# Optimization experiments

Hardware: AMD Instinct MI355X
Metric: run time of the kernel (lower is better)

The kernel has to match this reference:

```python
import jax, jax.numpy as jnp
import numpy as np

# Config / sizes
N = 20000       # nodes
E = 320000      # edges (avg degree 16)
IN_DIM = 6      # node feature dim
PE = 8          # laplacian PE dims
ED = 4          # edge feature dim
H = 128         # hidden dim
OUT = 4         # output dim
L = 3           # message-passing layers
T = 3           # node types (typed encoders/decoders)


def mlp(z, W1, b1, W2, b2):
    # _make_mlp: Linear -> ReLU -> Linear
    return jax.nn.relu(z @ W1 + b1) @ W2 + b2


def typed_mlp(z, W1, b1, W2, b2, types):
    # W1: [T, Din, H]; compute all T branches, select per-node by type
    h = jax.nn.relu(jnp.einsum('ni,tih->tnh', z, W1) + b1[:, None, :])
    o = jnp.einsum('tnh,tho->tno', h, W2) + b2[:, None, :]
    onehot = jax.nn.one_hot(types, W1.shape[0], dtype=o.dtype)  # [N, T]
    return jnp.einsum('tno,nt->no', o, onehot)


def setup_inputs() -> dict:
    key = jax.random.key(0)
    ks = jax.random.split(key, 40)

    def w(k, shape, fan_in):
        return jax.random.normal(k, shape, dtype=jnp.float32) / np.float32(np.sqrt(fan_in))

    inp = {}
    inp['x'] = jax.random.normal(ks[0], (N, IN_DIM), dtype=jnp.float32)
    inp['pe'] = jax.random.normal(ks[1], (N, PE), dtype=jnp.float32)
    inp['edge_attr'] = jax.random.normal(ks[2], (E, ED), dtype=jnp.float32)
    # typed node encoders: (in_dim+pe_dims) -> H -> H
    inp['enc_W1'] = w(ks[3], (T, IN_DIM + PE, H), IN_DIM + PE)
    inp['enc_b1'] = jnp.zeros((T, H), jnp.float32)
    inp['enc_W2'] = w(ks[4], (T, H, H), H)
    inp['enc_b2'] = jnp.zeros((T, H), jnp.float32)
    # edge encoder: ED -> H -> H
    inp['ee_W1'] = w(ks[5], (ED, H), ED)
    inp['ee_b1'] = jnp.zeros((H,), jnp.float32)
    inp['ee_W2'] = w(ks[6], (H, H), H)
    inp['ee_b2'] = jnp.zeros((H,), jnp.float32)
    # per-layer edge update (3H->H->H), node update (2H->H->H), fusion (H->H->H)
    inp['eu_W1'] = w(ks[7], (L, 3 * H, H), 3 * H)
    inp['eu_b1'] = jnp.zeros((L, H), jnp.float32)
    inp['eu_W2'] = w(ks[8], (L, H, H), H)
    inp['eu_b2'] = jnp.zeros((L, H), jnp.float32)
    inp['nu_W1'] = w(ks[9], (L, 2 * H, H), 2 * H)
    inp['nu_b1'] = jnp.zeros((L, H), jnp.float32)
    inp['nu_W2'] = w(ks[10], (L, H, H), H)
    inp['nu_b2'] = jnp.zeros((L, H), jnp.float32)
    inp['fu_W1'] = w(ks[11], (L, H, H), H)
    inp['fu_b1'] = jnp.zeros((L, H), jnp.float32)
    inp['fu_W2'] = w(ks[12], (L, H, H), H)
    inp['fu_b2'] = jnp.zeros((L, H), jnp.float32)
    # typed decoders: H -> H -> OUT
    inp['dec_W1'] = w(ks[13], (T, H, H), H)
    inp['dec_b1'] = jnp.zeros((T, H), jnp.float32)
    inp['dec_W2'] = w(ks[14], (T, H, OUT), H)
    inp['dec_b2'] = jnp.zeros((T, OUT), jnp.float32)
    # int inputs
    inp['edge_index'] = jax.random.randint(ks[15], (2, E), 0, N)
    inp['node_types'] = jax.random.randint(ks[16], (N,), 0, T)
    return inp


def reference(x, pe, edge_attr,
              enc_W1, enc_b1, enc_W2, enc_b2,
              ee_W1, ee_b1, ee_W2, ee_b2,
              eu_W1, eu_b1, eu_W2, eu_b2,
              nu_W1, nu_b1, nu_W2, nu_b2,
              fu_W1, fu_b1, fu_W2, fu_b2,
              dec_W1, dec_b1, dec_W2, dec_b2,
              edge_index, node_types):
    n = x.shape[0]
    src, dst = edge_index[0], edge_index[1]
    # typed node encode on [x || pe]
    h_nodes = typed_mlp(jnp.concatenate([x, pe], axis=-1),
                        enc_W1, enc_b1, enc_W2, enc_b2, node_types)
    # edge encode
    h_edges = mlp(edge_attr, ee_W1, ee_b1, ee_W2, ee_b2)
    num_layers = eu_W1.shape[0]
    for l in range(num_layers):
        # gather endpoint states, edge MLP, residual on edges
        m_edge = mlp(jnp.concatenate([h_nodes[src], h_nodes[dst], h_edges], axis=-1),
                     eu_W1[l], eu_b1[l], eu_W2[l], eu_b2[l])
        h_edges = h_edges + m_edge
        # scatter-add aggregation to destination nodes (index_add_)
        m_node = jax.ops.segment_sum(h_edges, dst, num_segments=n)
        # node update + residual, then fusion (dropout is eval/identity)
        upd = mlp(jnp.concatenate([h_nodes, m_node], axis=-1),
                  nu_W1[l], nu_b1[l], nu_W2[l], nu_b2[l])
        local = h_nodes + upd
        h_nodes = mlp(local, fu_W1[l], fu_b1[l], fu_W2[l], fu_b2[l])
    # typed decode
    out = typed_mlp(h_nodes, dec_W1, dec_b1, dec_W2, dec_b2, node_types)
    return out
```

## Files before the change

### kernel.cpp

```cpp
#include <hip/hip_runtime.h>
#include <hip/hip_bf16.h>

typedef __hip_bfloat16 bf16;
typedef __attribute__((ext_vector_type(8))) short short8;
typedef __attribute__((ext_vector_type(4))) float floatx4;

#define HDIM 128
#define NCANON 27

__device__ __forceinline__ float b2f(bf16 v) { return __bfloat162float(v); }
__device__ __forceinline__ float s2f(short s) {
  return __uint_as_float(((unsigned int)(unsigned short)s) << 16);
}
__device__ __forceinline__ short f2s(float f) {
  return (short)__bfloat16_as_ushort(__float2bfloat16(f));
}

__global__ void detect_kernel(const unsigned short* __restrict__ xraw, int* __restrict__ flag) {
  int j = threadIdx.x;
  unsigned short u = xraw[2 * j];
  int e = (u >> 7) & 0xFF;
  int ok = (u == 0) || (e >= 100 && e <= 140);
  unsigned long long m = __ballot(ok);
  if (j == 0) flag[0] = (__popcll(m) >= 48) ? 1 : 0;
}

struct CanonDesc {
  const void* src[NCANON];
  int prefix[NCANON + 1];
};

__global__ void canon_kernel(CanonDesc d, const int* __restrict__ flag,
                             bf16* __restrict__ out, int total) {
  int t = blockIdx.x * 256 + threadIdx.x;
  if (t >= total) return;
  int ti = 0;
  while (d.prefix[ti + 1] <= t) ti++;
  int off = t - d.prefix[ti];
  if (flag[0]) out[t] = ((const bf16*)d.src[ti])[off];
  else         out[t] = __float2bfloat16(((const float*)d.src[ti])[off]);
}

__global__ void emit_kernel(const bf16* __restrict__ canon_out, const int* __restrict__ flag,
                            void* __restrict__ d_out, int n) {
  int t = blockIdx.x * 256 + threadIdx.x;
  if (t >= n) return;
  if (flag[0]) ((bf16*)d_out)[t] = canon_out[t];
  else         ((float*)d_out)[t] = __bfloat162float(canon_out[t]);
}

__global__ void hist_kernel(const int* __restrict__ dst, int* __restrict__ cnt, int E) {
  int e = blockIdx.x * 256 + threadIdx.x;
  if (e < E) atomicAdd(&cnt[dst[e]], 1);
}

__global__ void scan1_kernel(const int* __restrict__ cnt, int* __restrict__ bsum, int n) {
  int tid = threadIdx.x, lane = tid & 63, wave = tid >> 6;
  int i = blockIdx.x * 256 + tid;
  int v = (i < n) ? cnt[i] : 0;
  #pragma unroll
  for (int d = 32; d; d >>= 1) v += __shfl_down(v, d);
  __shared__ int ws[4];
  if (lane == 0) ws[wave] = v;
  __syncthreads();
  if (tid == 0) bsum[blockIdx.x] = ws[0] + ws[1] + ws[2] + ws[3];
}

__global__ void scan2_kernel(int* __restrict__ bsum, int nb) {
  int lane = threadIdx.x;
  int a0 = (lane < nb) ? bsum[lane] : 0;
  int b0 = (64 + lane < nb) ? bsum[64 + lane] : 0;
  int a = a0, b = b0;
  #pragma unroll
  for (int d = 1; d < 64; d <<= 1) { int t = __shfl_up(a, d); if (lane >= d) a += t; }
  int totA = __shfl(a, 63);
  #pragma unroll
  for (int d = 1; d < 64; d <<= 1) { int t = __shfl_up(b, d); if (lane >= d) b += t; }
  int totB = __shfl(b, 63);
  if (lane < nb) bsum[lane] = a - a0;
  if (64 + lane < nb) bsum[64 + lane] = b - b0 + totA;
  if (lane == 0) bsum[nb] = totA + totB;
}

__global__ void scan3_kernel(const int* __restrict__ cnt, const int* __restrict__ bsum,
                             int* __restrict__ row_start, int n, int nb) {
  __shared__ int sh[256];
  int tid = threadIdx.x;
  int i = blockIdx.x * 256 + tid;
  int v = (i < n) ? cnt[i] : 0;
  sh[tid] = v;
  __syncthreads();
  #pragma unroll
  for (int off = 1; off < 256; off <<= 1) {
    int t = (tid >= off) ? sh[tid - off] : 0;
    __syncthreads();
    sh[tid] += t;
    __syncthreads();
  }
  if (i < n) row_start[i] = bsum[blockIdx.x] + sh[tid] - v;
  if (blockIdx.x == 0 && tid == 0) row_start[n] = bsum[nb];
}

__global__ void scatter_kernel(const int* __restrict__ src, const int* __restrict__ dst,
                               const int* __restrict__ row_start, int* __restrict__ cursor,
                               int* __restrict__ sortedE, int* __restrict__ srcS,
                               int* __restrict__ dstS, int E) {
  int e = blockIdx.x * 256 + threadIdx.x;
  if (e < E) {
    int d = dst[e];
    int pos = row_start[d] + atomicAdd(&cursor[d], 1);
    sortedE[pos] = e;
    srcS[pos] = src[e];
    dstS[pos] = d;
  }
}

__global__ void tcount_kernel(const int* __restrict__ types, int* __restrict__ bcnt, int n) {
  int i = blockIdx.x * 256 + threadIdx.x;
  int lane = threadIdx.x & 63, wave = threadIdx.x >> 6;
  int t = (i < n) ? types[i] : -1;
  __shared__ int wc[4][3];
  unsigned long long m0 = __ballot(t == 0);
  unsigned long long m1 = __ballot(t == 1);
  unsigned long long m2 = __ballot(t == 2);
  if (lane == 0) {
    wc[wave][0] = __popcll(m0); wc[wave][1] = __popcll(m1); wc[wave][2] = __popcll(m2);
  }
  __syncthreads();
  if (threadIdx.x < 3)
    bcnt[blockIdx.x * 3 + threadIdx.x] =
        wc[0][threadIdx.x] + wc[1][threadIdx.x] + wc[2][threadIdx.x] + wc[3][threadIdx.x];
}

__global__ void tscan_kernel(const int* __restrict__ bcnt, int* __restrict__ boff,
                             int* __restrict__ ts, int nb, int n) {
  int lane = threadIdx.x;
  __shared__ int tots[3];
  for (int t = 0; t < 3; t++) {
    int a0 = (lane < nb) ? bcnt[lane * 3 + t] : 0;
    int b0 = (64 + lane < nb) ? bcnt[(64 + lane) * 3 + t] : 0;
    int a = a0, b = b0;
    #pragma unroll
    for (int d = 1; d < 64; d <<= 1) { int x = __shfl_up(a, d); if (lane >= d) a += x; }
    int totA = __shfl(a, 63);
    #pragma unroll
    for (int d = 1; d < 64; d <<= 1) { int x = __shfl_up(b, d); if (lane >= d) b += x; }
    int totB = __shfl(b, 63);
    if (lane < nb) boff[lane * 3 + t] = a - a0;
    if (64 + lane < nb) boff[(64 + lane) * 3 + t] = b - b0 + totA;
    if (lane == 0) tots[t] = totA + totB;
  }
  __syncthreads();
  int tot0 = tots[0], tot1 = tots[1];
  if (lane == 0) { ts[0] = 0; ts[1] = tot0; ts[2] = tot0 + tot1; ts[3] = n; }
  for (int idx = lane; idx < nb; idx += 64) {
    boff[idx * 3 + 1] += tot0;
    boff[idx * 3 + 2] += tot0 + tot1;
  }
}

__global__ void tscatter2_kernel(const int* __restrict__ types, const int* __restrict__ boff,
                                 int* __restrict__ perm, int n) {
  int i = blockIdx.x * 256 + threadIdx.x;
  int lane = threadIdx.x & 63, wave = threadIdx.x >> 6;
  int t = (i < n) ? types[i] : -1;
  __shared__ int wc[4][3];
  unsigned long long m0 = __ballot(t == 0);
  unsigned long long m1 = __ballot(t == 1);
  unsigned long long m2 = __ballot(t == 2);
  if (lane == 0) {
    wc[wave][0] = __popcll(m0); wc[wave][1] = __popcll(m1); wc[wave][2] = __popcll(m2);
  }
  __syncthreads();
  if (i >= n) return;
  unsigned long long mt = (t == 0) ? m0 : ((t == 1) ? m1 : m2);
  unsigned long long below = (lane == 0) ? 0ull : ((1ull << lane) - 1ull);
  int laneRank = __popcll(mt & below);
  int waveOff = 0;
  for (int w = 0; w < wave; w++) waveOff += wc[w][t];
  perm[boff[blockIdx.x * 3 + t] + waveOff + laneRank] = i;
}

struct PackJob { const bf16* src; bf16* dst; int Ksrc; int KS; int srcCols; };
struct PackJobs { PackJob j[40]; };

__global__ void pack_all_kernel(PackJobs J) {
  PackJob job = J.j[blockIdx.y];
  int idx = blockIdx.x * 256 + threadIdx.x;
  int total = 8 * job.KS * 64;
  if (idx >= total) return;
  int lane = idx & 63;
  int ks = (idx >> 6) % job.KS;
  int ct = idx / (64 * job.KS);
  bf16* o = job.dst + (size_t)idx * 8;
  int ncol = ct * 16 + (lane & 15);
  int kb = ks * 32 + ((lane >> 4) & 3) * 8;
  #pragma unroll
  for (int jj = 0; jj < 8; jj++) {
    int k = kb + jj;
    o[jj] = (k < job.Ksrc && ncol < job.srcCols)
              ? job.src[(size_t)k * job.srcCols + ncol] : __float2bfloat16(0.f);
  }
}

__global__ void __launch_bounds__(256) ygemm_kernel(
    const bf16* __restrict__ X,
    const bf16* __restrict__ WpA, const bf16* __restrict__ WpB,
    bf16* __restrict__ outA, bf16* __restrict__ outB, int M) {
  const bf16* Wp = blockIdx.y ? WpB : WpA;
  bf16* outp = blockIdx.y ? outB : outA;
  constexpr int BM = 64, RT = 4, SK = 136;
  __shared__ bf16 Zt[BM * SK];
  const int tid = threadIdx.x;
  const int lane = tid & 63, wave = tid >> 6, colq = lane & 15, quad = lane >> 4;
  const int row0 = blockIdx.x * BM;
  {
    int row = tid >> 2, sub = tid & 3;
    int gr = row0 + row;
    bool ok = gr < M;
    #pragma unroll
    for (int j = 0; j < 4; j++) {
      int seg = j * 4 + sub;
      uint4 v = {0u, 0u, 0u, 0u};
      if (ok) v = *(const uint4*)(X + (size_t)gr * HDIM + seg * 8);
      *(uint4*)(&Zt[row * SK + seg * 8]) = v;
    }
  }
  __syncthreads();
  floatx4 acc[RT][2];
  #pragma unroll
  for (int rt = 0; rt < RT; rt++)
    #pragma unroll
    for (int c = 0; c < 2; c++) acc[rt][c] = (floatx4){0.f, 0.f, 0.f, 0.f};
  #pragma unroll
  for (int ks = 0; ks < 4; ks++) {
    short8 bfr0 = *(const short8*)(Wp + (((size_t)(wave * 2 + 0) * 4 + ks) * 64 + lane) * 8);
    short8 bfr1 = *(const short8*)(Wp + (((size_t)(wave * 2 + 1) * 4 + ks) * 64 + lane) * 8);
    #pragma unroll
    for (int rt = 0; rt < RT; rt++) {
      short8 a = *(const short8*)(&Zt[(rt * 16 + colq) * SK + ks * 32 + quad * 8]);
      acc[rt][0] = __builtin_amdgcn_mfma_f32_16x16x32_bf16(a, bfr0, acc[rt][0], 0, 0, 0);
      acc[rt][1] = __builtin_amdgcn_mfma_f32_16x16x32_bf16(a, bfr1, acc[rt][1], 0, 0, 0);
    }
  }
  #pragma unroll
  for (int c = 0; c < 2; c++) {
    int col = wave * 32 + c * 16 + colq;
    #pragma unroll
    for (int rt = 0; rt < RT; rt++)
      #pragma unroll
      for (int r = 0; r < 4; r++) {
        int grow = row0 + rt * 16 + quad * 4 + r;
        if (grow < M) outp[(size_t)grow * HDIM + col] = __float2bfloat16(acc[rt][c][r]);
      }
  }
}

template<int BM>
__global__ void __launch_bounds__(256) eu_kernel(
    const bf16* __restrict__ he, const bf16* __restrict__ ysrc, const bf16* __restrict__ ydst,
    const int* __restrict__ srcS, const int* __restrict__ dstS,
    const bf16* __restrict__ W1p, const bf16* __restrict__ b1v,
    const bf16* __restrict__ W2p, const bf16* __restrict__ b2v,
    bf16* __restrict__ outp, float* __restrict__ mnode, int M) {
  constexpr int RT = BM / 16;
  constexpr int SK = 264;
  __shared__ bf16 Zt[BM * SK];
  __shared__ int dstLds[BM];
  const int tid = threadIdx.x;
  const int lane = tid & 63, wave = tid >> 6, colq = lane & 15, quad = lane >> 4;
  const int row0 = blockIdx.x * BM;
  constexpr int TPR = 256 / BM;
  {
    int row = tid / TPR, sub = tid % TPR;
    int gr = row0 + row;
    bool ok = gr < M;
    int g0 = ok ? srcS[gr] : 0;
    int g1 = ok ? dstS[gr] : 0;
    if (sub == 0) dstLds[row] = ok ? g1 : -1;
    #pragma unroll
    for (int j = 0; j < 32 / TPR; j++) {
      int c = j * TPR + sub;
      int part = c >> 4, seg = c & 15;
      if (part == 0) {
        short8 o = {0, 0, 0, 0, 0, 0, 0, 0};
        if (ok) {
          short8 a = *(const short8*)(ysrc + (size_t)g0 * HDIM + seg * 8);
          short8 b = *(const short8*)(ydst + (size_t)g1 * HDIM + seg * 8);
          #pragma unroll
          for (int k = 0; k < 8; k++) o[k] = f2s(s2f(a[k]) + s2f(b[k]));
        }
        *(short8*)(&Zt[row * SK + seg * 8]) = o;
      } else {
        uint4 v = {0u, 0u, 0u, 0u};
        if (ok) v = *(const uint4*)(he + (size_t)gr * HDIM + seg * 8);
        *(uint4*)(&Zt[row * SK + 128 + seg * 8]) = v;
      }
    }
  }
  __syncthreads();

  floatx4 acc[RT][2];
  #pragma unroll
  for (int rt = 0; rt < RT; rt++)
    #pragma unroll
    for (int c = 0; c < 2; c++) acc[rt][c] = (floatx4){0.f, 0.f, 0.f, 0.f};
  #pragma unroll
  for (int ks = 0; ks < 4; ks++) {
    short8 bfr0 = *(const short8*)(W1p + (((size_t)(wave * 2 + 0) * 4 + ks) * 64 + lane) * 8);
    short8 bfr1 = *(const short8*)(W1p + (((size_t)(wave * 2 + 1) * 4 + ks) * 64 + lane) * 8);
    #pragma unroll
    for (int rt = 0; rt < RT; rt++) {
      short8 a = *(const short8*)(&Zt[(rt * 16 + colq) * SK + 128 + ks * 32 + quad * 8]);
      acc[rt][0] = __builtin_amdgcn_mfma_f32_16x16x32_bf16(a, bfr0, acc[rt][0], 0, 0, 0);
      acc[rt][1] = __builtin_amdgcn_mfma_f32_16x16x32_bf16(a, bfr1, acc[rt][1], 0, 0, 0);
    }
  }
  #pragma unroll
  for (int c = 0; c < 2; c++) {
    int col = wave * 32 + c * 16 + colq;
    float bv = b2f(b1v[col]);
    #pragma unroll
    for (int rt = 0; rt < RT; rt++)
      #pragma unroll
      for (int r = 0; r < 4; r++) {
        int lrow = rt * 16 + quad * 4 + r;
        float v = acc[rt][c][r] + bv + b2f(Zt[lrow * SK + col]);
        Zt[lrow * SK + col] = __float2bfloat16(fmaxf(v, 0.f));
      }
  }
  __syncthreads();

  floatx4 acc2[RT][2];
  #pragma unroll
  for (int rt = 0; rt < RT; rt++)
    #pragma unroll
    for (int c = 0; c < 2; c++) acc2[rt][c] = (floatx4){0.f, 0.f, 0.f, 0.f};
  #pragma unroll
  for (int ks = 0; ks < 4; ks++) {
    short8 bfr0 = *(const short8*)(W2p + (((size_t)(wave * 2 + 0) * 4 + ks) * 64 + lane) * 8);
    short8 bfr1 = *(const short8*)(W2p + (((size_t)(wave * 2 + 1) * 4 + ks) * 64 + lane) * 8);
    #pragma unroll
    for (int rt = 0; rt < RT; rt++) {
      short8 a = *(const short8*)(&Zt[(rt * 16 + colq) * SK + ks * 32 + quad * 8]);
      acc2[rt][0] = __builtin_amdgcn_mfma_f32_16x16x32_bf16(a, bfr0, acc2[rt][0], 0, 0, 0);
      acc2[rt][1] = __builtin_amdgcn_mfma_f32_16x16x32_bf16(a, bfr1, acc2[rt][1], 0, 0, 0);
    }
  }
  #pragma unroll
  for (int c = 0; c < 2; c++) {
    int col = wave * 32 + c * 16 + colq;
    float bv = b2f(b2v[col]);
    #pragma unroll
    for (int rt = 0; rt < RT; rt++)
      #pragma unroll
      for (int r = 0; r < 4; r++) {
        int lrow = rt * 16 + quad * 4 + r;
        int grow = row0 + lrow;
        float v = acc2[rt][c][r] + bv + b2f(Zt[lrow * SK + 128 + col]);
        bf16 vb = __float2bfloat16(v);
        Zt[lrow * SK + 128 + col] = vb;
        if (grow < M) outp[(size_t)grow * HDIM + col] = vb;
      }
  }
  __syncthreads();

  if (tid < 128) {
    int col = tid;
    float s = 0.f;
    int runDst = dstLds[0];
    bool touchStart = true;
    for (int r = 0; r < BM; r++) {
      int d = dstLds[r];
      if (d != runDst) {
        if (runDst >= 0) {
          float* mp = &mnode[(size_t)runDst * HDIM + col];
          if (touchStart) atomicAdd(mp, s); else *mp = s;
        }
        runDst = d; s = 0.f; touchStart = false;
      }
      s += b2f(Zt[r * SK + 128 + col]);
    }
    if (runDst >= 0) atomicAdd(&mnode[(size_t)runDst * HDIM + col], s);
  }
}

__global__ void __launch_bounds__(256) node_kernel(
    const bf16* __restrict__ h_nodes, const float* __restrict__ mnode,
    const bf16* __restrict__ nuW1, const bf16* __restrict__ nuB1,
    const bf16* __restrict__ nuW2, const bf16* __restrict__ nuB2,
    const bf16* __restrict__ fuW1, const bf16* __restrict__ fuB1,
    const bf16* __restrict__ fuW2, const bf16* __restrict__ fuB2,
    bf16* __restrict__ outp, int M) {
  constexpr int BM = 64, RT = 4, SK = 264;
  __shared__ bf16 Zt[BM * SK];
  const int tid = threadIdx.x;
  const int lane = tid & 63, wave = tid >> 6, colq = lane & 15, quad = lane >> 4;
  const int row0 = blockIdx.x * BM;
  {
    int row = tid >> 2, sub = tid & 3;
    int gr = row0 + row;
    bool ok = gr < M;
    #pragma unroll
    for (int j = 0; j < 8; j++) {
      int c = j * 4 + sub;
      int part = c >> 4, seg = c & 15;
      if (part == 0) {
        uint4 v = {0u, 0u, 0u, 0u};
        if (ok) v = *(const uint4*)(h_nodes + (size_t)gr * HDIM + seg * 8);
        *(uint4*)(&Zt[row * SK + seg * 8]) = v;
      } else {
        short8 o = {0, 0, 0, 0, 0, 0, 0, 0};
        if (ok) {
          const float* mp = mnode + (size_t)gr * HDIM + seg * 8;
          #pragma unroll
          for (int k = 0; k < 8; k++) o[k] = f2s(mp[k]);
        }
        *(short8*)(&Zt[row * SK + 128 + seg * 8]) = o;
      }
    }
  }
  __syncthreads();

  floatx4 acc[RT][2];
  #pragma unroll
  for (int rt = 0; rt < RT; rt++)
    #pragma unroll
    for (int c = 0; c < 2; c++) acc[rt][c] = (floatx4){0.f, 0.f, 0.f, 0.f};
  #pragma unroll
  for (int ks = 0; ks < 8; ks++) {
    short8 bfr0 = *(const short8*)(nuW1 + (((size_t)(wave * 2 + 0) * 8 + ks) * 64 + lane) * 8);
    short8 bfr1 = *(const short8*)(nuW1 + (((size_t)(wave * 2 + 1) * 8 + ks) * 64 + lane) * 8);
    #pragma unroll
    for (int rt = 0; rt < RT; rt++) {
      short8 a = *(const short8*)(&Zt[(rt * 16 + colq) * SK + ks * 32 + quad * 8]);
      acc[rt][0] = __builtin_amdgcn_mfma_f32_16x16x32_bf16(a, bfr0, acc[rt][0], 0, 0, 0);
      acc[rt][1] = __builtin_amdgcn_mfma_f32_16x16x32_bf16(a, bfr1, acc[rt][1], 0, 0, 0);
    }
  }
  __syncthreads();
  #pragma unroll
  for (int c = 0; c < 2; c++) {
    int col = wave * 32 + c * 16 + colq;
    float bv = b2f(nuB1[col]);
    #pragma unroll
    for (int rt = 0; rt < RT; rt++)
      #pragma unroll
      for (int r = 0; r < 4; r++)
        Zt[(rt * 16 + quad * 4 + r) * SK + 128 + col] =
            __float2bfloat16(fmaxf(acc[rt][c][r] + bv, 0.f));
  }
  __syncthreads();

  #pragma unroll
  for (int rt = 0; rt < RT; rt++)
    #pragma unroll
    for (int c = 0; c < 2; c++) acc[rt][c] = (floatx4){0.f, 0.f, 0.f, 0.f};
  #pragma unroll
  for (int ks = 0; ks < 4; ks++) {
    short8 bfr0 = *(const short8*)(nuW2 + (((size_t)(wave * 2 + 0) * 4 + ks) * 64 + lane) * 8);
    short8 bfr1 = *(const short8*)(nuW2 + (((size_t)(wave * 2 + 1) * 4 + ks) * 64 + lane) * 8);
    #pragma unroll
    for (int rt = 0; rt < RT; rt++) {
      short8 a = *(const short8*)(&Zt[(rt * 16 + colq) * SK + 128 + ks * 32 + quad * 8]);
      acc[rt][0] = __builtin_amdgcn_mfma_f32_16x16x32_bf16(a, bfr0, acc[rt][0], 0, 0, 0);
      acc[rt][1] = __builtin_amdgcn_mfma_f32_16x16x32_bf16(a, bfr1, acc[rt][1], 0, 0, 0);
    }
  }
  #pragma unroll
  for (int c = 0; c < 2; c++) {
    int col = wave * 32 + c * 16 + colq;
    float bv = b2f(nuB2[col]);
    #pragma unroll
    for (int rt = 0; rt < RT; rt++)
      #pragma unroll
      for (int r = 0; r < 4; r++) {
        int lrow = rt * 16 + quad * 4 + r;
        float v = acc[rt][c][r] + bv + b2f(Zt[lrow * SK + col]);
        Zt[lrow * SK + col] = __float2bfloat16(v);
      }
  }
  __syncthreads();

  #pragma unroll
  for (int rt = 0; rt < RT; rt++)
    #pragma unroll
    for (int c = 0; c < 2; c++) acc[rt][c] = (floatx4){0.f, 0.f, 0.f, 0.f};
  #pragma unroll
  for (int ks = 0; ks < 4; ks++) {
    short8 bfr0 = *(const short8*)(fuW1 + (((size_t)(wave * 2 + 0) * 4 + ks) * 64 + lane) * 8);
    short8 bfr1 = *(const short8*)(fuW1 + (((size_t)(wave * 2 + 1) * 4 + ks) * 64 + lane) * 8);
    #pragma unroll
    for (int rt = 0; rt < RT; rt++) {
      short8 a = *(const short8*)(&Zt[(rt * 16 + colq) * SK + ks * 32 + quad * 8]);
      acc[rt][0] = __builtin_amdgcn_mfma_f32_16x16x32_bf16(a, bfr0, acc[rt][0], 0, 0, 0);
      acc[rt][1] = __builtin_amdgcn_mfma_f32_16x16x32_bf16(a, bfr1, acc[rt][1], 0, 0, 0);
    }
  }
  #pragma unroll
  for (int c = 0; c < 2; c++) {
    int col = wave * 32 + c * 16 + colq;
    float bv = b2f(fuB1[col]);
    #pragma unroll
    for (int rt = 0; rt < RT; rt++)
      #pragma unroll
      for (int r = 0; r < 4; r++)
        Zt[(rt * 16 + quad * 4 + r) * SK + 128 + col] =
            __float2bfloat16(fmaxf(acc[rt][c][r] + bv, 0.f));
  }
  __syncthreads();

  #pragma unroll
  for (int rt = 0; rt < RT; rt++)
    #pragma unroll
    for (int c = 0; c < 2; c++) acc[rt][c] = (floatx4){0.f, 0.f, 0.f, 0.f};
  #pragma unroll
  for (int ks = 0; ks < 4; ks++) {
    short8 bfr0 = *(const short8*)(fuW2 + (((size_t)(wave * 2 + 0) * 4 + ks) * 64 + lane) * 8);
    short8 bfr1 = *(const short8*)(fuW2 + (((size_t)(wave * 2 + 1) * 4 + ks) * 64 + lane) * 8);
    #pragma unroll
    for (int rt = 0; rt < RT; rt++) {
      short8 a = *(const short8*)(&Zt[(rt * 16 + colq) * SK + 128 + ks * 32 + quad * 8]);
      acc[rt][0] = __builtin_amdgcn_mfma_f32_16x16x32_bf16(a, bfr0, acc[rt][0], 0, 0, 0);
      acc[rt][1] = __builtin_amdgcn_mfma_f32_16x16x32_bf16(a, bfr1, acc[rt][1], 0, 0, 0);
    }
  }
  #pragma unroll
  for (int c = 0; c < 2; c++) {
    int col = wave * 32 + c * 16 + colq;
    float bv = b2f(fuB2[col]);
    #pragma unroll
    for (int rt = 0; rt < RT; rt++)
      #pragma unroll
      for (int r = 0; r < 4; r++) {
        int grow = row0 + rt * 16 + quad * 4 + r;
        if (grow < M) outp[(size_t)grow * HDIM + col] = __float2bfloat16(acc[rt][c][r] + bv);
      }
  }
}

template<int KS1, bool DEC>
__global__ void __launch_bounds__(256) typed_kernel(
    const bf16* __restrict__ in0, const bf16* __restrict__ in1,
    const int* __restrict__ perm, const int* __restrict__ ts,
    const bf16* __restrict__ W1p, int w1s, const bf16* __restrict__ b1v, int b1s,
    const bf16* __restrict__ W2p, int w2s, const bf16* __restrict__ b2v, int b2s,
    bf16* __restrict__ outp) {
  constexpr int BM = 64, RT = 4;
  constexpr int SK = KS1 * 32 + 8;
  constexpr int HS = 136;
  int t = blockIdx.y;
  int rs = ts[t], re = ts[t + 1];
  int row0 = rs + blockIdx.x * BM;
  if (row0 >= re) return;
  __shared__ bf16 Zt[BM * SK];
  __shared__ bf16 Hid[BM * HS];
  __shared__ int gIdx[BM];
  const int tid = threadIdx.x;
  const int lane = tid & 63, wave = tid >> 6, colq = lane & 15, quad = lane >> 4;
  for (int i = tid; i < BM; i += 256) gIdx[i] = (row0 + i < re) ? perm[row0 + i] : -1;
  __syncthreads();
  if (DEC) {
    int row = tid >> 2, sub = tid & 3;
    int g = gIdx[row];
    #pragma unroll
    for (int j = 0; j < 4; j++) {
      int seg = j * 4 + sub;
      uint4 v = {0u, 0u, 0u, 0u};
      if (g >= 0) v = *(const uint4*)(in0 + (size_t)g * HDIM + seg * 8);
      *(uint4*)(&Zt[row * SK + seg * 8]) = v;
    }
  } else {
    for (int i = tid; i < BM * 32; i += 256) {
      int row = i >> 5, k = i & 31;
      int g = gIdx[row];
      bf16 v = __float2bfloat16(0.f);
      if (g >= 0 && k < 14) v = (k < 6) ? in0[(size_t)g * 6 + k] : in1[(size_t)g * 8 + (k - 6)];
      Zt[row * SK + k] = v;
    }
  }
  __syncthreads();

  const bf16* W1t = W1p + (size_t)t * w1s;
  const bf16* W2t = W2p + (size_t)t * w2s;
  floatx4 acc[RT][2];
  #pragma unroll
  for (int rt = 0; rt < RT; rt++)
    #pragma unroll
    for (int c = 0; c < 2; c++) acc[rt][c] = (floatx4){0.f, 0.f, 0.f, 0.f};
  #pragma unroll
  for (int ks = 0; ks < KS1; ks++) {
    short8 bfr0 = *(const short8*)(W1t + (((size_t)(wave * 2 + 0) * KS1 + ks) * 64 + lane) * 8);
    short8 bfr1 = *(const short8*)(W1t + (((size_t)(wave * 2 + 1) * KS1 + ks) * 64 + lane) * 8);
    #pragma unroll
    for (int rt = 0; rt < RT; rt++) {
      short8 a = *(const short8*)(&Zt[(rt * 16 + colq) * SK + ks * 32 + quad * 8]);
      acc[rt][0] = __builtin_amdgcn_mfma_f32_16x16x32_bf16(a, bfr0, acc[rt][0], 0, 0, 0);
      acc[rt][1] = __builtin_amdgcn_mfma_f32_16x16x32_bf16(a, bfr1, acc[rt][1], 0, 0, 0);
    }
  }
  #pragma unroll
  for (int c = 0; c < 2; c++) {
    int col = wave * 32 + c * 16 + colq;
    float bv = b2f(b1v[t * b1s + col]);
    #pragma unroll
    for (int rt = 0; rt < RT; rt++)
      #pragma unroll
      for (int r = 0; r < 4; r++) {
        float v = acc[rt][c][r] + bv;
        Hid[(rt * 16 + quad * 4 + r) * HS + col] = __float2bfloat16(fmaxf(v, 0.f));
      }
  }
  __syncthreads();

  floatx4 acc2[RT][2];
  #pragma unroll
  for (int rt = 0; rt < RT; rt++)
    #pragma unroll
    for (int c = 0; c < 2; c++) acc2[rt][c] = (floatx4){0.f, 0.f, 0.f, 0.f};
  #pragma unroll
  for (int ks = 0; ks < 4; ks++) {
    short8 bfr0 = *(const short8*)(W2t + (((size_t)(wave * 2 + 0) * 4 + ks) * 64 + lane) * 8);
    short8 bfr1 = *(const short8*)(W2t + (((size_t)(wave * 2 + 1) * 4 + ks) * 64 + lane) * 8);
    #pragma unroll
    for (int rt = 0; rt < RT; rt++) {
      short8 a = *(const short8*)(&Hid[(rt * 16 + colq) * HS + ks * 32 + quad * 8]);
      acc2[rt][0] = __builtin_amdgcn_mfma_f32_16x16x32_bf16(a, bfr0, acc2[rt][0], 0, 0, 0);
      acc2[rt][1] = __builtin_amdgcn_mfma_f32_16x16x32_bf16(a, bfr1, acc2[rt][1], 0, 0, 0);
    }
  }
  if (DEC) {
    if (wave == 0 && colq < 4) {
      float bv = b2f(b2v[t * b2s + colq]);
      #pragma unroll
      for (int rt = 0; rt < RT; rt++)
        #pragma unroll
        for (int r = 0; r < 4; r++) {
          int g = gIdx[rt * 16 + quad * 4 + r];
          if (g >= 0) outp[(size_t)g * 4 + colq] = __float2bfloat16(acc2[rt][0][r] + bv);
        }
    }
  } else {
    #pragma unroll
    for (int c = 0; c < 2; c++) {
      int col = wave * 32 + c * 16 + colq;
      float bv = b2f(b2v[t * b2s + col]);
      #pragma unroll
      for (int rt = 0; rt < RT; rt++)
        #pragma unroll
        for (int r = 0; r < 4; r++) {
          int g = gIdx[rt * 16 + quad * 4 + r];
          if (g >= 0) outp[(size_t)g * HDIM + col] = __float2bfloat16(acc2[rt][c][r] + bv);
        }
    }
  }
}

template<int BM>
__global__ void __launch_bounds__(256) ee_kernel(
    const bf16* __restrict__ p0, const int* __restrict__ idx0,
    const bf16* __restrict__ W1p, const bf16* __restrict__ b1v,
    const bf16* __restrict__ W2p, const bf16* __restrict__ b2v,
    bf16* __restrict__ outp, int M) {
  constexpr int RT = BM / 16;
  constexpr int SK = 136;
  __shared__ bf16 Zt[BM * SK];
  const int tid = threadIdx.x;
  const int lane = tid & 63, wave = tid >> 6, colq = lane & 15, quad = lane >> 4;
  const int row0 = blockIdx.x * BM;

  for (int i = tid; i < BM * 4; i += 256) {
    int row = i >> 2, seg = i & 3;
    int gr = row0 + row;
    uint4 val = {0u, 0u, 0u, 0u};
    if (seg == 0 && gr < M) {
      int g = idx0 ? idx0[gr] : gr;
      uint2 v = *(const uint2*)(p0 + (size_t)g * 4);
      val.x = v.x; val.y = v.y;
    }
    *(uint4*)(&Zt[row * SK + seg * 8]) = val;
  }
  __syncthreads();

  floatx4 acc[RT][2];
  #pragma unroll
  for (int rt = 0; rt < RT; rt++)
    #pragma unroll
    for (int c = 0; c < 2; c++) acc[rt][c] = (floatx4){0.f, 0.f, 0.f, 0.f};
  {
    short8 bfr0 = *(const short8*)(W1p + (((size_t)(wave * 2 + 0)) * 64 + lane) * 8);
    short8 bfr1 = *(const short8*)(W1p + (((size_t)(wave * 2 + 1)) * 64 + lane) * 8);
    #pragma unroll
    for (int rt = 0; rt < RT; rt++) {
      short8 a = *(const short8*)(&Zt[(rt * 16 + colq) * SK + quad * 8]);
      acc[rt][0] = __builtin_amdgcn_mfma_f32_16x16x32_bf16(a, bfr0, acc[rt][0], 0, 0, 0);
      acc[rt][1] = __builtin_amdgcn_mfma_f32_16x16x32_bf16(a, bfr1, acc[rt][1], 0, 0, 0);
    }
  }
  __syncthreads();
  #pragma unroll
  for (int c = 0; c < 2; c++) {
    int col = wave * 32 + c * 16 + colq;
    float bv = b2f(b1v[col]);
    #pragma unroll
    for (int rt = 0; rt < RT; rt++)
      #pragma unroll
      for (int r = 0; r < 4; r++)
        Zt[(rt * 16 + quad * 4 + r) * SK + col] =
            __float2bfloat16(fmaxf(acc[rt][c][r] + bv, 0.f));
  }
  __syncthreads();

  floatx4 acc2[RT][2];
  #pragma unroll
  for (int rt = 0; rt < RT; rt++)
    #pragma unroll
    for (int c = 0; c < 2; c++) acc2[rt][c] = (floatx4){0.f, 0.f, 0.f, 0.f};
  #pragma unroll
  for (int ks = 0; ks < 4; ks++) {
    short8 bfr0 = *(const short8*)(W2p + (((size_t)(wave * 2 + 0) * 4 + ks) * 64 + lane) * 8);
    short8 bfr1 = *(const short8*)(W2p + (((size_t)(wave * 2 + 1) * 4 + ks) * 64 + lane) * 8);
    #pragma unroll
    for (int rt = 0; rt < RT; rt++) {
      short8 a = *(const short8*)(&Zt[(rt * 16 + colq) * SK + ks * 32 + quad * 8]);
      acc2[rt][0] = __builtin_amdgcn_mfma_f32_16x16x32_bf16(a, bfr0, acc2[rt][0], 0, 0, 0);
      acc2[rt][1] = __builtin_amdgcn_mfma_f32_16x16x32_bf16(a, bfr1, acc2[rt][1], 0, 0, 0);
    }
  }
  #pragma unroll
  for (int c = 0; c < 2; c++) {
    int col = wave * 32 + c * 16 + colq;
    float bv = b2f(b2v[col]);
    #pragma unroll
    for (int rt = 0; rt < RT; rt++)
      #pragma unroll
      for (int r = 0; r < 4; r++) {
        int grow = row0 + rt * 16 + quad * 4 + r;
        if (grow < M)
          outp[(size_t)grow * HDIM + col] = __float2bfloat16(acc2[rt][c][r] + bv);
      }
  }
}

extern "C" void kernel_launch(void* const* d_in, const int* in_sizes, int n_in,
                              void* d_out, int out_size, void* d_ws, size_t ws_size,
                              hipStream_t stream) {
  const int* edge_index = (const int*)d_in[27];
  const int* node_types = (const int*)d_in[28];
  const int N = in_sizes[28];
  const int E = in_sizes[2] / 4;
  const int L = in_sizes[12] / HDIM;
  const int* srcI = edge_index;
  const int* dstI = edge_index + E;

  CanonDesc cd;
  int total = 0;
  for (int i = 0; i < NCANON; i++) { cd.src[i] = d_in[i]; cd.prefix[i] = total; total += in_sizes[i]; }
  cd.prefix[NCANON] = total;

  char* wsb = (char*)d_ws;
  size_t off = 0;
  auto alloc = [&](size_t bytes) -> void* {
    void* p = wsb + off;
    off += (bytes + 255) & ~(size_t)255;
    return p;
  };
  int*  flag      = (int*)alloc(256);
  bf16* arena     = (bf16*)alloc((size_t)total * 2);
  bf16* h_nodes   = (bf16*)alloc((size_t)N * HDIM * 2);
  bf16* h_edges   = (bf16*)alloc((size_t)E * HDIM * 2);
  float* m_node   = (float*)alloc((size_t)N * HDIM * 4);
  bf16* ysrcb     = (bf16*)alloc((size_t)N * HDIM * 2);
  bf16* ydstb     = (bf16*)alloc((size_t)N * HDIM * 2);
  bf16* canon_out = (bf16*)alloc((size_t)out_size * 2);
  int* counts     = (int*)alloc((size_t)N * 4);
  int* cursor     = (int*)alloc((size_t)N * 4);
  int* row_start  = (int*)alloc((size_t)(N + 1) * 4);
  int* bsum       = (int*)alloc(260 * 4);
  int* sortedE    = (int*)alloc((size_t)E * 4);
  int* srcS       = (int*)alloc((size_t)E * 4);
  int* dstS       = (int*)alloc((size_t)E * 4);
  int* bcntT      = (int*)alloc(512 * 4);
  int* boffT      = (int*)alloc(512 * 4);
  int* tsArr      = (int*)alloc(64);
  int* permT      = (int*)alloc((size_t)N * 4);
  bf16* eeW1p  = (bf16*)alloc(4096 * 2);
  bf16* eeW2p  = (bf16*)alloc(16384 * 2);
  bf16* encW1p = (bf16*)alloc(3 * 4096 * 2);
  bf16* encW2p = (bf16*)alloc(3 * 16384 * 2);
  bf16* decW1p = (bf16*)alloc(3 * 16384 * 2);
  bf16* decW2p = (bf16*)alloc(3 * 16384 * 2);
  bf16* euW1a  = (bf16*)alloc((size_t)L * 16384 * 2);
  bf16* euW1b  = (bf16*)alloc((size_t)L * 16384 * 2);
  bf16* euW1c  = (bf16*)alloc((size_t)L * 16384 * 2);
  bf16* euW2p  = (bf16*)alloc((size_t)L * 16384 * 2);
  bf16* nuW1p  = (bf16*)alloc((size_t)L * 32768 * 2);
  bf16* nuW2p  = (bf16*)alloc((size_t)L * 16384 * 2);
  bf16* fuW1p  = (bf16*)alloc((size_t)L * 16384 * 2);
  bf16* fuW2p  = (bf16*)alloc((size_t)L * 16384 * 2);

  const bf16* cX     = arena + cd.prefix[0];
  const bf16* cPE    = arena + cd.prefix[1];
  const bf16* cEA    = arena + cd.prefix[2];
  const bf16* cEncW1 = arena + cd.prefix[3];
  const bf16* cEncB1 = arena + cd.prefix[4];
  const bf16* cEncW2 = arena + cd.prefix[5];
  const bf16* cEncB2 = arena + cd.prefix[6];
  const bf16* cEeW1  = arena + cd.prefix[7];
  const bf16* cEeB1  = arena + cd.prefix[8];
  const bf16* cEeW2  = arena + cd.prefix[9];
  const bf16* cEeB2  = arena + cd.prefix[10];
  const bf16* cEuW1  = arena + cd.prefix[11];
  const bf16* cEuB1  = arena + cd.prefix[12];
  const bf16* cEuW2  = arena + cd.prefix[13];
  const bf16* cEuB2  = arena + cd.prefix[14];
  const bf16* cNuW1  = arena + cd.prefix[15];
  const bf16* cNuB1  = arena + cd.prefix[16];
  const bf16* cNuW2  = arena + cd.prefix[17];
  const bf16* cNuB2  = arena + cd.prefix[18];
  const bf16* cFuW1  = arena + cd.prefix[19];
  const bf16* cFuB1  = arena + cd.prefix[20];
  const bf16* cFuW2  = arena + cd.prefix[21];
  const bf16* cFuB2  = arena + cd.prefix[22];
  const bf16* cDecW1 = arena + cd.prefix[23];
  const bf16* cDecB1 = arena + cd.prefix[24];
  const bf16* cDecW2 = arena + cd.prefix[25];
  const bf16* cDecB2 = arena + cd.prefix[26];

  detect_kernel<<<1, 64, 0, stream>>>((const unsigned short*)d_in[0], flag);
  canon_kernel<<<(total + 255) / 256, 256, 0, stream>>>(cd, flag, arena, total);

  hipMemsetAsync(counts, 0, (size_t)N * 4, stream);
  hipMemsetAsync(cursor, 0, (size_t)N * 4, stream);

  PackJobs PJ;
  int nj = 0;
  PJ.j[nj++] = {cEeW1, eeW1p, 4, 1, 128};
  PJ.j[nj++] = {cEeW2, eeW2p, 128, 4, 128};
  for (int l = 0; l < L; l++) {
    const bf16* w1 = cEuW1 + (size_t)l * 384 * HDIM;
    PJ.j[nj++] = {w1,                 euW1a + (size_t)l * 16384, 128, 4, 128};
    PJ.j[nj++] = {w1 + 128 * HDIM,    euW1b + (size_t)l * 16384, 128, 4, 128};
    PJ.j[nj++] = {w1 + 256 * HDIM,    euW1c + (size_t)l * 16384, 128, 4, 128};
    PJ.j[nj++] = {cEuW2 + (size_t)l * HDIM * HDIM, euW2p + (size_t)l * 16384, 128, 4, 128};
    PJ.j[nj++] = {cNuW1 + (size_t)l * 256 * HDIM,  nuW1p + (size_t)l * 32768, 256, 8, 128};
    PJ.j[nj++] = {cNuW2 + (size_t)l * HDIM * HDIM, nuW2p + (size_t)l * 16384, 128, 4, 128};
    PJ.j[nj++] = {cFuW1 + (size_t)l * HDIM * HDIM, fuW1p + (size_t)l * 16384, 128, 4, 128};
    PJ.j[nj++] = {cFuW2 + (size_t)l * HDIM * HDIM, fuW2p + (size_t)l * 16384, 128, 4, 128};
  }
  for (int t = 0; t < 3; t++) {
    PJ.j[nj++] = {cEncW1 + (size_t)t * 14 * HDIM,   encW1p + (size_t)t * 4096, 14, 1, 128};
    PJ.j[nj++] = {cEncW2 + (size_t)t * HDIM * HDIM, encW2p + (size_t)t * 16384, 128, 4, 128};
    PJ.j[nj++] = {cDecW1 + (size_t)t * HDIM * HDIM, decW1p + (size_t)t * 16384, 128, 4, 128};
    PJ.j[nj++] = {cDecW2 + (size_t)t * HDIM * 4,    decW2p + (size_t)t * 16384, 128, 4, 4};
  }
  pack_all_kernel<<<dim3(16, nj), 256, 0, stream>>>(PJ);

  int nb = (N + 255) / 256;
  hist_kernel<<<(E + 255) / 256, 256, 0, stream>>>(dstI, counts, E);
  scan1_kernel<<<nb, 256, 0, stream>>>(counts, bsum, N);
  scan2_kernel<<<1, 64, 0, stream>>>(bsum, nb);
  scan3_kernel<<<nb, 256, 0, stream>>>(counts, bsum, row_start, N, nb);
  scatter_kernel<<<(E + 255) / 256, 256, 0, stream>>>(srcI, dstI, row_start, cursor,
                                                      sortedE, srcS, dstS, E);
  tcount_kernel<<<nb, 256, 0, stream>>>(node_types, bcntT, N);
  tscan_kernel<<<1, 64, 0, stream>>>(bcntT, boffT, tsArr, nb, N);
  tscatter2_kernel<<<nb, 256, 0, stream>>>(node_types, boffT, permT, N);

  int ngrid64 = (N + 63) / 64;
  typed_kernel<1, false><<<dim3(ngrid64, 3), 256, 0, stream>>>(
      cX, cPE, permT, tsArr, encW1p, 4096, cEncB1, HDIM,
      encW2p, 16384, cEncB2, HDIM, h_nodes);

  int egrid32  = (E + 31) / 32;
  int egrid128 = (E + 127) / 128;

  ee_kernel<128><<<egrid128, 256, 0, stream>>>(
      cEA, sortedE, eeW1p, cEeB1, eeW2p, cEeB2, h_edges, E);

  for (int l = 0; l < L; l++) {
    hipMemsetAsync(m_node, 0, (size_t)N * HDIM * 4, stream);
    ygemm_kernel<<<dim3(ngrid64, 2), 256, 0, stream>>>(
        h_nodes, euW1a + (size_t)l * 16384, euW1b + (size_t)l * 16384, ysrcb, ydstb, N);
    eu_kernel<32><<<egrid32, 256, 0, stream>>>(
        h_edges, ysrcb, ydstb, srcS, dstS,
        euW1c + (size_t)l * 16384, cEuB1 + l * HDIM,
        euW2p + (size_t)l * 16384, cEuB2 + l * HDIM, h_edges, m_node, E);
    node_kernel<<<ngrid64, 256, 0, stream>>>(
        h_nodes, m_node,
        nuW1p + (size_t)l * 32768, cNuB1 + l * HDIM,
        nuW2p + (size_t)l * 16384, cNuB2 + l * HDIM,
        fuW1p + (size_t)l * 16384, cFuB1 + l * HDIM,
        fuW2p + (size_t)l * 16384, cFuB2 + l * HDIM, h_nodes, N);
  }

  typed_kernel<4, true><<<dim3(ngrid64, 3), 256, 0, stream>>>(
      h_nodes, nullptr, permT, tsArr, decW1p, 16384, cDecB1, HDIM,
      decW2p, 16384, cDecB2, 4, canon_out);
  emit_kernel<<<(out_size + 255) / 256, 256, 0, stream>>>(canon_out, flag, d_out, out_size);
  (void)n_in; (void)ws_size;
}
```

Baseline: 503.8 us.

## Fuse small setup kernels, fold memset into ygemm, store projections in fp32

Several small launches go away. Format detection moves into the canon kernel, the three type-sort kernels become one single-block sort, the emit kernel becomes a direct dtype-aware write from the decoder, and the per-layer m_node memset is folded into ygemm. The ygemm outputs change from bf16 to fp32, which doubles the gather traffic in eu_kernel but avoids a double rounding. The segment reduction in eu_kernel now uses all 256 threads split into two halves of rows. The single-block type sort serialises about 20 iterations with syncs.

```diff
diff --git a/kernel.cpp b/kernel.cpp
--- a/kernel.cpp
+++ b/kernel.cpp
@@ -14,15 +14,6 @@
 }
 __device__ __forceinline__ short f2s(float f) {
   return (short)__bfloat16_as_ushort(__float2bfloat16(f));
-}
-
-__global__ void detect_kernel(const unsigned short* __restrict__ xraw, int* __restrict__ flag) {
-  int j = threadIdx.x;
-  unsigned short u = xraw[2 * j];
-  int e = (u >> 7) & 0xFF;
-  int ok = (u == 0) || (e >= 100 && e <= 140);
-  unsigned long long m = __ballot(ok);
-  if (j == 0) flag[0] = (__popcll(m) >= 48) ? 1 : 0;
 }
 
 struct CanonDesc {
@@ -30,23 +21,27 @@
   int prefix[NCANON + 1];
 };
 
-__global__ void canon_kernel(CanonDesc d, const int* __restrict__ flag,
-                             bf16* __restrict__ out, int total) {
-  int t = blockIdx.x * 256 + threadIdx.x;
+__global__ void canon_kernel(CanonDesc d, const unsigned short* __restrict__ xraw,
+                             int* __restrict__ flagOut, bf16* __restrict__ out, int total) {
+  __shared__ int sflag;
+  int tid = threadIdx.x;
+  if (tid < 64) {
+    unsigned short u = xraw[2 * tid];
+    int e = (u >> 7) & 0xFF;
+    int ok = (u == 0) || (e >= 100 && e <= 140);
+    unsigned long long m = __ballot(ok);
+    if (tid == 0) sflag = (__popcll(m) >= 48) ? 1 : 0;
+  }
+  __syncthreads();
+  int isBf = sflag;
+  if (blockIdx.x == 0 && tid == 0) flagOut[0] = isBf;
+  int t = blockIdx.x * 256 + tid;
   if (t >= total) return;
-  int ti = 0;
-  while (d.prefix[ti + 1] <= t) ti++;
-  int off = t - d.prefix[ti];
-  if (flag[0]) out[t] = ((const bf16*)d.src[ti])[off];
-  else         out[t] = __float2bfloat16(((const float*)d.src[ti])[off]);
-}
-
-__global__ void emit_kernel(const bf16* __restrict__ canon_out, const int* __restrict__ flag,
-                            void* __restrict__ d_out, int n) {
-  int t = blockIdx.x * 256 + threadIdx.x;
-  if (t >= n) return;
-  if (flag[0]) ((bf16*)d_out)[t] = canon_out[t];
-  else         ((float*)d_out)[t] = __bfloat162float(canon_out[t]);
+  int lo = 0, hi = NCANON;
+  while (lo + 1 < hi) { int mid = (lo + hi) >> 1; if (d.prefix[mid] <= t) lo = mid; else hi = mid; }
+  int off = t - d.prefix[lo];
+  out[t] = isBf ? ((const bf16*)d.src[lo])[off]
+                : __float2bfloat16(((const float*)d.src[lo])[off]);
 }
 
 __global__ void hist_kernel(const int* __restrict__ dst, int* __restrict__ cnt, int E) {
@@ -115,70 +110,54 @@
   }
 }
 
-__global__ void tcount_kernel(const int* __restrict__ types, int* __restrict__ bcnt, int n) {
-  int i = blockIdx.x * 256 + threadIdx.x;
-  int lane = threadIdx.x & 63, wave = threadIdx.x >> 6;
-  int t = (i < n) ? types[i] : -1;
-  __shared__ int wc[4][3];
-  unsigned long long m0 = __ballot(t == 0);
-  unsigned long long m1 = __ballot(t == 1);
-  unsigned long long m2 = __ballot(t == 2);
-  if (lane == 0) {
-    wc[wave][0] = __popcll(m0); wc[wave][1] = __popcll(m1); wc[wave][2] = __popcll(m2);
-  }
-  __syncthreads();
-  if (threadIdx.x < 3)
-    bcnt[blockIdx.x * 3 + threadIdx.x] =
-        wc[0][threadIdx.x] + wc[1][threadIdx.x] + wc[2][threadIdx.x] + wc[3][threadIdx.x];
-}
-
-__global__ void tscan_kernel(const int* __restrict__ bcnt, int* __restrict__ boff,
-                             int* __restrict__ ts, int nb, int n) {
-  int lane = threadIdx.x;
-  __shared__ int tots[3];
-  for (int t = 0; t < 3; t++) {
-    int a0 = (lane < nb) ? bcnt[lane * 3 + t] : 0;
-    int b0 = (64 + lane < nb) ? bcnt[(64 + lane) * 3 + t] : 0;
-    int a = a0, b = b0;
-    #pragma unroll
-    for (int d = 1; d < 64; d <<= 1) { int x = __shfl_up(a, d); if (lane >= d) a += x; }
-    int totA = __shfl(a, 63);
-    #pragma unroll
-    for (int d = 1; d < 64; d <<= 1) { int x = __shfl_up(b, d); if (lane >= d) b += x; }
-    int totB = __shfl(b, 63);
-    if (lane < nb) boff[lane * 3 + t] = a - a0;
-    if (64 + lane < nb) boff[(64 + lane) * 3 + t] = b - b0 + totA;
-    if (lane == 0) tots[t] = totA + totB;
-  }
-  __syncthreads();
-  int tot0 = tots[0], tot1 = tots[1];
-  if (lane == 0) { ts[0] = 0; ts[1] = tot0; ts[2] = tot0 + tot1; ts[3] = n; }
-  for (int idx = lane; idx < nb; idx += 64) {
-    boff[idx * 3 + 1] += tot0;
-    boff[idx * 3 + 2] += tot0 + tot1;
-  }
-}
-
-__global__ void tscatter2_kernel(const int* __restrict__ types, const int* __restrict__ boff,
-                                 int* __restrict__ perm, int n) {
-  int i = blockIdx.x * 256 + threadIdx.x;
-  int lane = threadIdx.x & 63, wave = threadIdx.x >> 6;
-  int t = (i < n) ? types[i] : -1;
-  __shared__ int wc[4][3];
-  unsigned long long m0 = __ballot(t == 0);
-  unsigned long long m1 = __ballot(t == 1);
-  unsigned long long m2 = __ballot(t == 2);
-  if (lane == 0) {
-    wc[wave][0] = __popcll(m0); wc[wave][1] = __popcll(m1); wc[wave][2] = __popcll(m2);
-  }
-  __syncthreads();
-  if (i >= n) return;
-  unsigned long long mt = (t == 0) ? m0 : ((t == 1) ? m1 : m2);
-  unsigned long long below = (lane == 0) ? 0ull : ((1ull << lane) - 1ull);
-  int laneRank = __popcll(mt & below);
-  int waveOff = 0;
-  for (int w = 0; w < wave; w++) waveOff += wc[w][t];
-  perm[boff[blockIdx.x * 3 + t] + waveOff + laneRank] = i;
+__global__ void __launch_bounds__(1024) tsort_kernel(const int* __restrict__ types,
+                                                     int* __restrict__ ts,
+                                                     int* __restrict__ perm, int n) {
+  __shared__ int wc[16][3];
+  __shared__ int base[3];
+  int tid = threadIdx.x, lane = tid & 63, wave = tid >> 6;
+  int c0 = 0, c1 = 0, c2 = 0;
+  for (int i = tid; i < n; i += 1024) {
+    int t = types[i];
+    c0 += (t == 0); c1 += (t == 1); c2 += (t == 2);
+  }
+  #pragma unroll
+  for (int d = 32; d; d >>= 1) {
+    c0 += __shfl_down(c0, d); c1 += __shfl_down(c1, d); c2 += __shfl_down(c2, d);
+  }
+  if (lane == 0) { wc[wave][0] = c0; wc[wave][1] = c1; wc[wave][2] = c2; }
+  __syncthreads();
+  if (tid == 0) {
+    int t0 = 0, t1 = 0;
+    for (int w = 0; w < 16; w++) { t0 += wc[w][0]; t1 += wc[w][1]; }
+    ts[0] = 0; ts[1] = t0; ts[2] = t0 + t1; ts[3] = n;
+    base[0] = 0; base[1] = t0; base[2] = t0 + t1;
+  }
+  __syncthreads();
+  for (int i0 = 0; i0 < n; i0 += 1024) {
+    int i = i0 + tid;
+    int t = (i < n) ? types[i] : -1;
+    unsigned long long m0 = __ballot(t == 0);
+    unsigned long long m1 = __ballot(t == 1);
+    unsigned long long m2 = __ballot(t == 2);
+    if (lane == 0) { wc[wave][0] = __popcll(m0); wc[wave][1] = __popcll(m1); wc[wave][2] = __popcll(m2); }
+    __syncthreads();
+    if (i < n) {
+      unsigned long long mt = (t == 0) ? m0 : ((t == 1) ? m1 : m2);
+      unsigned long long below = (lane == 0) ? 0ull : ((1ull << lane) - 1ull);
+      int r = __popcll(mt & below);
+      int woff = 0;
+      for (int w = 0; w < wave; w++) woff += wc[w][t];
+      perm[base[t] + woff + r] = i;
+    }
+    __syncthreads();
+    if (tid == 0) {
+      int a0 = 0, a1 = 0, a2 = 0;
+      for (int w = 0; w < 16; w++) { a0 += wc[w][0]; a1 += wc[w][1]; a2 += wc[w][2]; }
+      base[0] += a0; base[1] += a1; base[2] += a2;
+    }
+    __syncthreads();
+  }
 }
 
 struct PackJob { const bf16* src; bf16* dst; int Ksrc; int KS; int srcCols; };
@@ -206,14 +185,23 @@
 __global__ void __launch_bounds__(256) ygemm_kernel(
     const bf16* __restrict__ X,
     const bf16* __restrict__ WpA, const bf16* __restrict__ WpB,
-    bf16* __restrict__ outA, bf16* __restrict__ outB, int M) {
+    float* __restrict__ outA, float* __restrict__ outB,
+    float* __restrict__ mnode, int M) {
   const bf16* Wp = blockIdx.y ? WpB : WpA;
-  bf16* outp = blockIdx.y ? outB : outA;
+  float* outp = blockIdx.y ? outB : outA;
   constexpr int BM = 64, RT = 4, SK = 136;
   __shared__ bf16 Zt[BM * SK];
   const int tid = threadIdx.x;
   const int lane = tid & 63, wave = tid >> 6, colq = lane & 15, quad = lane >> 4;
   const int row0 = blockIdx.x * BM;
+  if (blockIdx.y == 0) {
+    float4 z = {0.f, 0.f, 0.f, 0.f};
+    for (int i = tid; i < BM * 32; i += 256) {
+      int row = i >> 5, q = i & 31;
+      int gr = row0 + row;
+      if (gr < M) *(float4*)(mnode + (size_t)gr * HDIM + q * 4) = z;
+    }
+  }
   {
     int row = tid >> 2, sub = tid & 3;
     int gr = row0 + row;
@@ -251,14 +239,14 @@
       #pragma unroll
       for (int r = 0; r < 4; r++) {
         int grow = row0 + rt * 16 + quad * 4 + r;
-        if (grow < M) outp[(size_t)grow * HDIM + col] = __float2bfloat16(acc[rt][c][r]);
+        if (grow < M) outp[(size_t)grow * HDIM + col] = acc[rt][c][r];
       }
   }
 }
 
 template<int BM>
 __global__ void __launch_bounds__(256) eu_kernel(
-    const bf16* __restrict__ he, const bf16* __restrict__ ysrc, const bf16* __restrict__ ydst,
+    const bf16* __restrict__ he, const float* __restrict__ ysrc, const float* __restrict__ ydst,
     const int* __restrict__ srcS, const int* __restrict__ dstS,
     const bf16* __restrict__ W1p, const bf16* __restrict__ b1v,
     const bf16* __restrict__ W2p, const bf16* __restrict__ b2v,
@@ -285,10 +273,10 @@
       if (part == 0) {
         short8 o = {0, 0, 0, 0, 0, 0, 0, 0};
         if (ok) {
-          short8 a = *(const short8*)(ysrc + (size_t)g0 * HDIM + seg * 8);
-          short8 b = *(const short8*)(ydst + (size_t)g1 * HDIM + seg * 8);
+          const float* ap = ysrc + (size_t)g0 * HDIM + seg * 8;
+          const float* bp = ydst + (size_t)g1 * HDIM + seg * 8;
           #pragma unroll
-          for (int k = 0; k < 8; k++) o[k] = f2s(s2f(a[k]) + s2f(b[k]));
+          for (int k = 0; k < 8; k++) o[k] = f2s(ap[k] + bp[k]);
         }
         *(short8*)(&Zt[row * SK + seg * 8]) = o;
       } else {
@@ -365,12 +353,14 @@
   }
   __syncthreads();
 
-  if (tid < 128) {
-    int col = tid;
+  {
+    int col = tid & 127;
+    int half = tid >> 7;
+    int rbeg = half * (BM / 2), rend = rbeg + (BM / 2);
     float s = 0.f;
-    int runDst = dstLds[0];
+    int runDst = dstLds[rbeg];
     bool touchStart = true;
-    for (int r = 0; r < BM; r++) {
+    for (int r = rbeg; r < rend; r++) {
       int d = dstLds[r];
       if (d != runDst) {
         if (runDst >= 0) {
@@ -542,10 +532,10 @@
 template<int KS1, bool DEC>
 __global__ void __launch_bounds__(256) typed_kernel(
     const bf16* __restrict__ in0, const bf16* __restrict__ in1,
-    const int* __restrict__ perm, const int* __restrict__ ts,
+    const int* __restrict__ perm, const int* __restrict__ ts, const int* __restrict__ flagp,
     const bf16* __restrict__ W1p, int w1s, const bf16* __restrict__ b1v, int b1s,
     const bf16* __restrict__ W2p, int w2s, const bf16* __restrict__ b2v, int b2s,
-    bf16* __restrict__ outp) {
+    void* __restrict__ outp) {
   constexpr int BM = 64, RT = 4;
   constexpr int SK = KS1 * 32 + 8;
   constexpr int HS = 136;
@@ -631,13 +621,18 @@
   }
   if (DEC) {
     if (wave == 0 && colq < 4) {
+      int isBf = flagp[0];
       float bv = b2f(b2v[t * b2s + colq]);
       #pragma unroll
       for (int rt = 0; rt < RT; rt++)
         #pragma unroll
         for (int r = 0; r < 4; r++) {
           int g = gIdx[rt * 16 + quad * 4 + r];
-          if (g >= 0) outp[(size_t)g * 4 + colq] = __float2bfloat16(acc2[rt][0][r] + bv);
+          if (g >= 0) {
+            float v = acc2[rt][0][r] + bv;
+            if (isBf) ((bf16*)outp)[(size_t)g * 4 + colq] = __float2bfloat16(v);
+            else      ((float*)outp)[(size_t)g * 4 + colq] = v;
+          }
         }
     }
   } else {
@@ -650,7 +645,7 @@
         #pragma unroll
         for (int r = 0; r < 4; r++) {
           int g = gIdx[rt * 16 + quad * 4 + r];
-          if (g >= 0) outp[(size_t)g * HDIM + col] = __float2bfloat16(acc2[rt][c][r] + bv);
+          if (g >= 0) ((bf16*)outp)[(size_t)g * HDIM + col] = __float2bfloat16(acc2[rt][c][r] + bv);
         }
     }
   }
@@ -770,9 +765,8 @@
   bf16* h_nodes   = (bf16*)alloc((size_t)N * HDIM * 2);
   bf16* h_edges   = (bf16*)alloc((size_t)E * HDIM * 2);
   float* m_node   = (float*)alloc((size_t)N * HDIM * 4);
-  bf16* ysrcb     = (bf16*)alloc((size_t)N * HDIM * 2);
-  bf16* ydstb     = (bf16*)alloc((size_t)N * HDIM * 2);
-  bf16* canon_out = (bf16*)alloc((size_t)out_size * 2);
+  float* ysrcb    = (float*)alloc((size_t)N * HDIM * 4);
+  float* ydstb    = (float*)alloc((size_t)N * HDIM * 4);
   int* counts     = (int*)alloc((size_t)N * 4);
   int* cursor     = (int*)alloc((size_t)N * 4);
   int* row_start  = (int*)alloc((size_t)(N + 1) * 4);
@@ -780,8 +774,6 @@
   int* sortedE    = (int*)alloc((size_t)E * 4);
   int* srcS       = (int*)alloc((size_t)E * 4);
   int* dstS       = (int*)alloc((size_t)E * 4);
-  int* bcntT      = (int*)alloc(512 * 4);
-  int* boffT      = (int*)alloc(512 * 4);
   int* tsArr      = (int*)alloc(64);
   int* permT      = (int*)alloc((size_t)N * 4);
   bf16* eeW1p  = (bf16*)alloc(4096 * 2);
@@ -827,8 +819,8 @@
   const bf16* cDecW2 = arena + cd.prefix[25];
   const bf16* cDecB2 = arena + cd.prefix[26];
 
-  detect_kernel<<<1, 64, 0, stream>>>((const unsigned short*)d_in[0], flag);
-  canon_kernel<<<(total + 255) / 256, 256, 0, stream>>>(cd, flag, arena, total);
+  canon_kernel<<<(total + 255) / 256, 256, 0, stream>>>(
+      cd, (const unsigned short*)d_in[0], flag, arena, total);
 
   hipMemsetAsync(counts, 0, (size_t)N * 4, stream);
   hipMemsetAsync(cursor, 0, (size_t)N * 4, stream);
@@ -863,13 +855,11 @@
   scan3_kernel<<<nb, 256, 0, stream>>>(counts, bsum, row_start, N, nb);
   scatter_kernel<<<(E + 255) / 256, 256, 0, stream>>>(srcI, dstI, row_start, cursor,
                                                       sortedE, srcS, dstS, E);
-  tcount_kernel<<<nb, 256, 0, stream>>>(node_types, bcntT, N);
-  tscan_kernel<<<1, 64, 0, stream>>>(bcntT, boffT, tsArr, nb, N);
-  tscatter2_kernel<<<nb, 256, 0, stream>>>(node_types, boffT, permT, N);
+  tsort_kernel<<<1, 1024, 0, stream>>>(node_types, tsArr, permT, N);
 
   int ngrid64 = (N + 63) / 64;
   typed_kernel<1, false><<<dim3(ngrid64, 3), 256, 0, stream>>>(
-      cX, cPE, permT, tsArr, encW1p, 4096, cEncB1, HDIM,
+      cX, cPE, permT, tsArr, flag, encW1p, 4096, cEncB1, HDIM,
       encW2p, 16384, cEncB2, HDIM, h_nodes);
 
   int egrid32  = (E + 31) / 32;
@@ -879,9 +869,8 @@
       cEA, sortedE, eeW1p, cEeB1, eeW2p, cEeB2, h_edges, E);
 
   for (int l = 0; l < L; l++) {
-    hipMemsetAsync(m_node, 0, (size_t)N * HDIM * 4, stream);
     ygemm_kernel<<<dim3(ngrid64, 2), 256, 0, stream>>>(
-        h_nodes, euW1a + (size_t)l * 16384, euW1b + (size_t)l * 16384, ysrcb, ydstb, N);
+        h_nodes, euW1a + (size_t)l * 16384, euW1b + (size_t)l * 16384, ysrcb, ydstb, m_node, N);
     eu_kernel<32><<<egrid32, 256, 0, stream>>>(
         h_edges, ysrcb, ydstb, srcS, dstS,
         euW1c + (size_t)l * 16384, cEuB1 + l * HDIM,
@@ -895,8 +884,7 @@
   }
 
   typed_kernel<4, true><<<dim3(ngrid64, 3), 256, 0, stream>>>(
-      h_nodes, nullptr, permT, tsArr, decW1p, 16384, cDecB1, HDIM,
-      decW2p, 16384, cDecB2, 4, canon_out);
-  emit_kernel<<<(out_size + 255) / 256, 256, 0, stream>>>(canon_out, flag, d_out, out_size);
+      h_nodes, nullptr, permT, tsArr, flag, decW1p, 16384, cDecB1, HDIM,
+      decW2p, 16384, cDecB2, 4, d_out);
   (void)n_in; (void)ws_size;
 }
```

New measurement: 527.4 us. 1.05x slower.
